# Kernel optimization log

Hardware: AMD Instinct MI355X
Metric: run time of the kernel (lower is better)

## Reference

```python
import jax, jax.numpy as jnp
import numpy as np

B, S, E, H = 1, 2048, 1024, 16
D = E // H  # head_dim = 64


def setup_inputs() -> dict:
    key = jax.random.key(0)
    ks = jax.random.split(key, 9)
    sd = 0.02
    hidden_states = jax.random.normal(ks[0], (B, S, E), dtype=jnp.float32)
    # causal mask: positions with mask==0 are filled with -inf (per masked_fill_)
    mask = jnp.tril(jnp.ones((1, 1, S, S), dtype=bool))
    Wq = jax.random.normal(ks[1], (E, E), dtype=jnp.float32) * sd
    bq = jax.random.normal(ks[2], (E,), dtype=jnp.float32) * sd
    Wk = jax.random.normal(ks[3], (D, E), dtype=jnp.float32) * sd
    bk = jax.random.normal(ks[4], (D,), dtype=jnp.float32) * sd
    Wv = jax.random.normal(ks[5], (D, E), dtype=jnp.float32) * sd
    bv = jax.random.normal(ks[6], (D,), dtype=jnp.float32) * sd
    Wo = jax.random.normal(ks[7], (E, E), dtype=jnp.float32) * sd
    bo = jax.random.normal(ks[8], (E,), dtype=jnp.float32) * sd
    return {"hidden_states": hidden_states, "mask": mask,
            "Wq": Wq, "bq": bq, "Wk": Wk, "bk": bk,
            "Wv": Wv, "bv": bv, "Wo": Wo, "bo": bo}


def reference(hidden_states, mask, Wq, bq, Wk, bk, Wv, bv, Wo, bo):
    bsz, tgt_len, embed_dim = hidden_states.shape
    # projections (torch Linear: x @ W^T + b)
    q = hidden_states @ Wq.T + bq                       # [B, S, E]
    q = q.reshape(bsz, tgt_len, H, D).transpose(0, 2, 1, 3)  # [B, H, S, D]
    k = hidden_states @ Wk.T + bk                       # [B, S, D] shared single KV head
    v = hidden_states @ Wv.T + bv                       # [B, S, D]
    scaling = jnp.sqrt(jnp.asarray(D, dtype=hidden_states.dtype))
    # QK^T with implicit broadcast of the shared K head (instead of expand)
    scores = jnp.einsum('bhqd,bkd->bhqk', q, k) / scaling   # [B, H, S, S]
    scores = jnp.where(mask, scores, -jnp.inf)
    probs = jax.nn.softmax(scores, axis=-1)             # dropout p=0 -> identity
    attn = jnp.einsum('bhqk,bkd->bhqd', probs, v)       # [B, H, S, D]
    attn = attn.transpose(0, 2, 1, 3).reshape(bsz, tgt_len, H * D)
    return attn @ Wo.T + bo                             # [B, S, E]
```

## Files before the change

### kernel.cpp

```cpp
#include <hip/hip_runtime.h>
#include <hip/hip_bf16.h>

typedef __hip_bfloat16 bf16;
typedef __attribute__((ext_vector_type(8))) short short8;
typedef __attribute__((ext_vector_type(4))) float f32x4;

__device__ __forceinline__ short8 ld8(const void* p) { return *(const short8*)p; }

__device__ __forceinline__ void async_cp16(bf16* lds, const bf16* g) {
    __builtin_amdgcn_global_load_lds(
        (const __attribute__((address_space(1))) unsigned int*)g,
        (__attribute__((address_space(3))) unsigned int*)lds, 16, 0, 0);
}

struct bf4 { bf16 a, b, c, d; };

__global__ void cast_kernel(const float* __restrict__ s0, bf16* __restrict__ d0, int n0_,
                            const float* __restrict__ s1, bf16* __restrict__ d1, int n1_,
                            const float* __restrict__ s2, bf16* __restrict__ d2, int n2_,
                            const float* __restrict__ s3, bf16* __restrict__ d3, int n3_,
                            const float* __restrict__ s4, bf16* __restrict__ d4, int n4_) {
    const float* srcs[5] = {s0, s1, s2, s3, s4};
    bf16* dsts[5] = {d0, d1, d2, d3, d4};
    int ns[5] = {n0_, n1_, n2_, n3_, n4_};
    int stride = gridDim.x * blockDim.x;
    int t0 = blockIdx.x * blockDim.x + threadIdx.x;
#pragma unroll
    for (int a = 0; a < 5; ++a) {
        const float4* src = (const float4*)srcs[a];
        bf4* dst = (bf4*)dsts[a];
        int n4 = ns[a] >> 2;
        for (int i = t0; i < n4; i += stride) {
            float4 v = src[i];
            bf4 o = {__float2bfloat16(v.x), __float2bfloat16(v.y),
                     __float2bfloat16(v.z), __float2bfloat16(v.w)};
            dst[i] = o;
        }
    }
}

#define GEMM_STAGE(dst, src_base, row0, ldk)                                   \
    _Pragma("unroll")                                                          \
    for (int u = 0; u < 4; ++u) {                                              \
        int t = wave * 4 + u;                                                  \
        int row = t * 4 + (lane >> 4);                                         \
        int gsrc = (lane & 15) ^ (row & 15);                                   \
        async_cp16(&dst[t * 4][0], src_base + (size_t)(row0 + row) * ldk + k0 + gsrc * 8); \
    }

__global__ void qkv_proj_kernel(const bf16* __restrict__ A,
                                const bf16* __restrict__ Wq, const bf16* __restrict__ Wk,
                                const bf16* __restrict__ Wv,
                                const float* __restrict__ bq, const float* __restrict__ bk,
                                const float* __restrict__ bv,
                                bf16* __restrict__ qo, bf16* __restrict__ ko,
                                bf16* __restrict__ vto, int M, int K) {
    __shared__ __align__(16) bf16 As[64][128];
    __shared__ __align__(16) bf16 Bs[64][128];
    const int nt = blockIdx.x;
    const bf16* W;
    const float* bias;
    int mode, nw0;
    if (nt < 16)      { W = Wq; bias = bq; mode = 0; nw0 = nt * 64; }
    else if (nt == 16){ W = Wk; bias = bk; mode = 1; nw0 = 0; }
    else              { W = Wv; bias = bv; mode = 2; nw0 = 0; }

    const int tid = threadIdx.x;
    const int wave = tid >> 6, lane = tid & 63;
    const int l16 = lane & 15, quad = lane >> 4;
    const int m0 = blockIdx.y * 64;

    f32x4 acc[4];
    const f32x4 z = {0.f, 0.f, 0.f, 0.f};
#pragma unroll
    for (int ni = 0; ni < 4; ++ni) acc[ni] = z;

    for (int k0 = 0; k0 < K; k0 += 128) {
        GEMM_STAGE(As, A, m0, K)
        GEMM_STAGE(Bs, W, nw0, K)
        __syncthreads();

        short8 af[4], bfr[4][4];
        {
            int R = wave * 16 + l16;
#pragma unroll
            for (int kc = 0; kc < 4; ++kc)
                af[kc] = ld8(&As[R][((kc * 4 + quad) ^ (R & 15)) * 8]);
        }
#pragma unroll
        for (int ni = 0; ni < 4; ++ni) {
            int r = ni * 16 + l16;
#pragma unroll
            for (int kc = 0; kc < 4; ++kc)
                bfr[kc][ni] = ld8(&Bs[r][((kc * 4 + quad) ^ (r & 15)) * 8]);
        }
#pragma unroll
        for (int kc = 0; kc < 4; ++kc)
#pragma unroll
            for (int ni = 0; ni < 4; ++ni)
                acc[ni] = __builtin_amdgcn_mfma_f32_16x16x32_bf16(
                    af[kc], bfr[kc][ni], acc[ni], 0, 0, 0);
        __syncthreads();
    }

#pragma unroll
    for (int ni = 0; ni < 4; ++ni)
#pragma unroll
        for (int r = 0; r < 4; ++r) {
            int row = m0 + wave * 16 + quad * 4 + r;
            int col = ni * 16 + l16;
            float v = acc[ni][r] + bias[nw0 + col];
            if (mode == 0)
                qo[(size_t)row * 1024 + nt * 64 + col] = __float2bfloat16(v * 0.125f);
            else if (mode == 1)
                ko[(size_t)row * 64 + col] = __float2bfloat16(v);
            else
                vto[(size_t)col * M + row] = __float2bfloat16(v);
        }
}

__global__ void gemm_bt_mfma(const bf16* __restrict__ A, const bf16* __restrict__ W,
                             const float* __restrict__ bias, float* __restrict__ C,
                             int M, int N, int K) {
    __shared__ __align__(16) bf16 As[64][128];
    __shared__ __align__(16) bf16 Bs[64][128];
    const int tid = threadIdx.x;
    const int wave = tid >> 6, lane = tid & 63;
    const int l16 = lane & 15, quad = lane >> 4;
    const int m0 = blockIdx.y * 64, n0 = blockIdx.x * 64;

    f32x4 acc[4];
    const f32x4 z = {0.f, 0.f, 0.f, 0.f};
#pragma unroll
    for (int ni = 0; ni < 4; ++ni) acc[ni] = z;

    for (int k0 = 0; k0 < K; k0 += 128) {
        GEMM_STAGE(As, A, m0, K)
        GEMM_STAGE(Bs, W, n0, K)
        __syncthreads();

        short8 af[4], bfr[4][4];
        {
            int R = wave * 16 + l16;
#pragma unroll
            for (int kc = 0; kc < 4; ++kc)
                af[kc] = ld8(&As[R][((kc * 4 + quad) ^ (R & 15)) * 8]);
        }
#pragma unroll
        for (int ni = 0; ni < 4; ++ni) {
            int r = ni * 16 + l16;
#pragma unroll
            for (int kc = 0; kc < 4; ++kc)
                bfr[kc][ni] = ld8(&Bs[r][((kc * 4 + quad) ^ (r & 15)) * 8]);
        }
#pragma unroll
        for (int kc = 0; kc < 4; ++kc)
#pragma unroll
            for (int ni = 0; ni < 4; ++ni)
                acc[ni] = __builtin_amdgcn_mfma_f32_16x16x32_bf16(
                    af[kc], bfr[kc][ni], acc[ni], 0, 0, 0);
        __syncthreads();
    }

#pragma unroll
    for (int ni = 0; ni < 4; ++ni)
#pragma unroll
        for (int r = 0; r < 4; ++r) {
            int row = m0 + wave * 16 + quad * 4 + r;
            int col = n0 + ni * 16 + l16;
            C[(size_t)row * N + col] = acc[ni][r] + bias[col];
        }
}

__global__ void flash_mfma_kernel(const bf16* __restrict__ Q, const bf16* __restrict__ Kg,
                                  const bf16* __restrict__ VT,
                                  bf16* __restrict__ Opart, float* __restrict__ Lpart,
                                  bf16* __restrict__ attn, int S) {
    const int s = blockIdx.x;
    int i, c;
    if (s < 32)      { c = 0; i = s; }
    else if (s < 56) { c = 1; i = s - 24; }
    else if (s < 72) { c = 2; i = s - 40; }
    else             { c = 3; i = s - 48; }

    __shared__ __align__(16) bf16 Ks[64][64];
    __shared__ __align__(16) bf16 Vt[64][64];
    __shared__ bf16 Ps[4][16][68];

    const int h = blockIdx.y;
    const int q0 = i * 64;
    const int tid = threadIdx.x;
    const int wave = tid >> 6, lane = tid & 63;
    const int l16 = lane & 15, quad = lane >> 4;
    const int lr = lane >> 3, lsw = (lane & 7) ^ (lr & 7);
    const int qrow = q0 + wave * 16;

    short8 qf[2];
#pragma unroll
    for (int kc = 0; kc < 2; ++kc)
        qf[kc] = ld8(Q + (size_t)(qrow + l16) * 1024 + h * 64 + kc * 32 + quad * 8);

    short8 onesf;
    {
        short o = (l16 == 0) ? (short)0x3F80 : (short)0;
        onesf[0]=o; onesf[1]=o; onesf[2]=o; onesf[3]=o;
        onesf[4]=o; onesf[5]=o; onesf[6]=o; onesf[7]=o;
    }

    f32x4 of[4];
    const f32x4 z = {0.f, 0.f, 0.f, 0.f};
#pragma unroll
    for (int dt = 0; dt < 4; ++dt) of[dt] = z;
    f32x4 lacc = z;

    const int jt0 = c * 8;
    const int jt1 = min(c * 8 + 8, i + 1);

    for (int jt = jt0; jt < jt1; ++jt) {
        const int j0 = jt * 64;
#pragma unroll
        for (int u = 0; u < 2; ++u) {
            int t = wave * 2 + u;
            async_cp16(&Ks[t * 8][0], Kg + (size_t)(j0 + t * 8 + lr) * 64 + lsw * 8);
            async_cp16(&Vt[t * 8][0], VT + (size_t)(t * 8 + lr) * S + j0 + lsw * 8);
        }
        __syncthreads();

        f32x4 sc[4];
#pragma unroll
        for (int nt = 0; nt < 4; ++nt) {
            int R = nt * 16 + l16;
            sc[nt] = __builtin_amdgcn_mfma_f32_16x16x32_bf16(
                qf[0], ld8(&Ks[R][(quad ^ (R & 7)) * 8]), z, 0, 0, 0);
            sc[nt] = __builtin_amdgcn_mfma_f32_16x16x32_bf16(
                qf[1], ld8(&Ks[R][((4 + quad) ^ (R & 7)) * 8]), sc[nt], 0, 0, 0);
        }
        bool need_mask = (j0 + 63 > qrow);
        if (need_mask) {
#pragma unroll
            for (int nt = 0; nt < 4; ++nt)
#pragma unroll
                for (int r = 0; r < 4; ++r)
                    if (j0 + nt * 16 + l16 > qrow + quad * 4 + r) sc[nt][r] = -1e30f;
        }

#pragma unroll
        for (int nt = 0; nt < 4; ++nt)
#pragma unroll
            for (int r = 0; r < 4; ++r)
                Ps[wave][quad * 4 + r][nt * 16 + l16] = __float2bfloat16(__expf(sc[nt][r]));

        short8 pf[2];
        pf[0] = ld8(&Ps[wave][l16][quad * 8]);
        pf[1] = ld8(&Ps[wave][l16][32 + quad * 8]);

        lacc = __builtin_amdgcn_mfma_f32_16x16x32_bf16(pf[0], onesf, lacc, 0, 0, 0);
        lacc = __builtin_amdgcn_mfma_f32_16x16x32_bf16(pf[1], onesf, lacc, 0, 0, 0);

#pragma unroll
        for (int dt = 0; dt < 4; ++dt) {
            int R = dt * 16 + l16;
            of[dt] = __builtin_amdgcn_mfma_f32_16x16x32_bf16(
                pf[0], ld8(&Vt[R][(quad ^ (R & 7)) * 8]), of[dt], 0, 0, 0);
            of[dt] = __builtin_amdgcn_mfma_f32_16x16x32_bf16(
                pf[1], ld8(&Vt[R][((4 + quad) ^ (R & 7)) * 8]), of[dt], 0, 0, 0);
        }
        __syncthreads();
    }

    if (s < 8) {
        float inv[4];
#pragma unroll
        for (int r = 0; r < 4; ++r)
            inv[r] = 1.f / __shfl(lacc[r], quad * 16);
#pragma unroll
        for (int dt = 0; dt < 4; ++dt)
#pragma unroll
            for (int r = 0; r < 4; ++r) {
                int row = q0 + wave * 16 + quad * 4 + r;
                attn[(size_t)row * 1024 + h * 64 + dt * 16 + l16] =
                    __float2bfloat16(of[dt][r] * inv[r]);
            }
        return;
    }

    bf16* Op = Opart + ((size_t)s * 16 + h) * 4096;
#pragma unroll
    for (int dt = 0; dt < 4; ++dt)
#pragma unroll
        for (int r = 0; r < 4; ++r) {
            int row = wave * 16 + quad * 4 + r;
            Op[row * 64 + dt * 16 + l16] = __float2bfloat16(of[dt][r]);
        }
    if (l16 == 0) {
        float* L = Lpart + ((size_t)s * 16 + h) * 64;
#pragma unroll
        for (int r = 0; r < 4; ++r)
            L[wave * 16 + quad * 4 + r] = lacc[r];
    }
}

__global__ void flash_merge_kernel(const bf16* __restrict__ Opart,
                                   const float* __restrict__ Lpart,
                                   bf16* __restrict__ attn) {
    const int i = blockIdx.x + 8, h = blockIdx.y;
    const int nch = (i >> 3) + 1;
    const int tid = threadIdx.x;
    const int row = tid >> 2, cg = (tid & 3) * 16;

    float L = 0.f;
    for (int cc = 0; cc < nch; ++cc) {
        int s = (cc == 0) ? i : (cc == 1) ? 24 + i : (cc == 2) ? 40 + i : 48 + i;
        L += Lpart[((size_t)s * 16 + h) * 64 + row];
    }
    float inv = 1.f / L;

    float o[16];
#pragma unroll
    for (int j = 0; j < 16; ++j) o[j] = 0.f;
    for (int cc = 0; cc < nch; ++cc) {
        int s = (cc == 0) ? i : (cc == 1) ? 24 + i : (cc == 2) ? 40 + i : 48 + i;
        const bf16* Op = Opart + ((size_t)s * 16 + h) * 4096 + row * 64 + cg;
#pragma unroll
        for (int j = 0; j < 16; ++j) o[j] += __bfloat162float(Op[j]);
    }
    bf16* dst = attn + (size_t)(i * 64 + row) * 1024 + h * 64 + cg;
#pragma unroll
    for (int j = 0; j < 16; ++j) dst[j] = __float2bfloat16(o[j] * inv);
}

extern "C" void kernel_launch(void* const* d_in, const int* in_sizes, int n_in,
                              void* d_out, int out_size, void* d_ws, size_t ws_size,
                              hipStream_t stream) {
    const int S = 2048, E = 1024, D = 64;

    const float* hs = (const float*)d_in[0];
    const float* Wq = (const float*)d_in[2];
    const float* bq = (const float*)d_in[3];
    const float* Wk = (const float*)d_in[4];
    const float* bk = (const float*)d_in[5];
    const float* Wv = (const float*)d_in[6];
    const float* bv = (const float*)d_in[7];
    const float* Wo = (const float*)d_in[8];
    const float* bo = (const float*)d_in[9];
    float* out = (float*)d_out;

    bf16* ws = (bf16*)d_ws;
    bf16* hsb = ws;
    bf16* wqb = hsb + (size_t)S * E;
    bf16* wkb = wqb + (size_t)E * E;
    bf16* wvb = wkb + (size_t)D * E;
    bf16* wob = wvb + (size_t)D * E;
    bf16* q = wob + (size_t)E * E;
    bf16* kbuf = q + (size_t)S * E;
    bf16* vt = kbuf + (size_t)S * D;
    bf16* attn = vt + (size_t)S * D;
    bf16* Opart = attn + (size_t)S * E;
    float* Lpart = (float*)(Opart + (size_t)1280 * 4096);

    cast_kernel<<<512, 256, 0, stream>>>(hs, hsb, S * E,
                                         Wq, wqb, E * E,
                                         Wk, wkb, D * E,
                                         Wv, wvb, D * E,
                                         Wo, wob, E * E);
    qkv_proj_kernel<<<dim3(18, S / 64), 256, 0, stream>>>(hsb, wqb, wkb, wvb,
                                                          bq, bk, bv,
                                                          q, kbuf, vt, S, E);
    flash_mfma_kernel<<<dim3(80, 16), 256, 0, stream>>>(q, kbuf, vt, Opart, Lpart, attn, S);
    flash_merge_kernel<<<dim3(24, 16), 256, 0, stream>>>(Opart, Lpart, attn);
    gemm_bt_mfma<<<dim3(E / 64, S / 64), 256, 0, stream>>>(attn, wob, bo, out, S, E, E);
}
```

Baseline: 147.9 us.

## Double-buffer LDS and widen N tile to 128 in projection GEMMs

Both projection GEMMs now double-buffer the A and B LDS tiles, so the next K slice is loaded asynchronously while MFMAs run on the current one. The N tile grows from 64 to 128 and each wave computes a 32x64 sub-tile, which raises operand reuse from LDS. The QKV kernel merges the K and V heads into one 128-wide tile. The cost is more LDS per block (96KB) and more accumulator registers, and the grids shrink to 9x32 and 8x32 blocks, which may underfill the CUs.

```diff
diff --git a/kernel.cpp b/kernel.cpp
--- a/kernel.cpp
+++ b/kernel.cpp
@@ -39,14 +39,31 @@
     }
 }
 
-#define GEMM_STAGE(dst, src_base, row0, ldk)                                   \
-    _Pragma("unroll")                                                          \
-    for (int u = 0; u < 4; ++u) {                                              \
-        int t = wave * 4 + u;                                                  \
-        int row = t * 4 + (lane >> 4);                                         \
-        int gsrc = (lane & 15) ^ (row & 15);                                   \
-        async_cp16(&dst[t * 4][0], src_base + (size_t)(row0 + row) * ldk + k0 + gsrc * 8); \
-    }
+template<int NROWS>
+__device__ __forceinline__ void stage_tile(bf16 (*dst)[128], const bf16* src,
+                                           int ldk, int wave, int lane) {
+#pragma unroll
+    for (int u = 0; u < NROWS / 16; ++u) {
+        int t = wave * (NROWS / 16) + u;
+        int row = t * 4 + (lane >> 4);
+        int gsrc = (lane & 15) ^ (row & 15);
+        async_cp16(&dst[t * 4][0], src + (size_t)row * ldk + gsrc * 8);
+    }
+}
+
+__device__ __forceinline__ void stage_kv(bf16 (*dst)[128], const bf16* Wk,
+                                         const bf16* Wv, int k0, int K,
+                                         int wave, int lane) {
+#pragma unroll
+    for (int u = 0; u < 8; ++u) {
+        int t = wave * 8 + u;
+        int row = t * 4 + (lane >> 4);
+        const bf16* src = (t < 16) ? (Wk + (size_t)row * K)
+                                   : (Wv + (size_t)(row - 64) * K);
+        int gsrc = (lane & 15) ^ (row & 15);
+        async_cp16(&dst[t * 4][0], src + k0 + gsrc * 8);
+    }
+}
 
 __global__ void qkv_proj_kernel(const bf16* __restrict__ A,
                                 const bf16* __restrict__ Wq, const bf16* __restrict__ Wk,
@@ -55,121 +72,152 @@
                                 const float* __restrict__ bv,
                                 bf16* __restrict__ qo, bf16* __restrict__ ko,
                                 bf16* __restrict__ vto, int M, int K) {
-    __shared__ __align__(16) bf16 As[64][128];
-    __shared__ __align__(16) bf16 Bs[64][128];
+    __shared__ __align__(16) bf16 As[2][64][128];
+    __shared__ __align__(16) bf16 Bs[2][128][128];
     const int nt = blockIdx.x;
-    const bf16* W;
-    const float* bias;
-    int mode, nw0;
-    if (nt < 16)      { W = Wq; bias = bq; mode = 0; nw0 = nt * 64; }
-    else if (nt == 16){ W = Wk; bias = bk; mode = 1; nw0 = 0; }
-    else              { W = Wv; bias = bv; mode = 2; nw0 = 0; }
-
+    const int m0 = blockIdx.y * 64;
     const int tid = threadIdx.x;
     const int wave = tid >> 6, lane = tid & 63;
     const int l16 = lane & 15, quad = lane >> 4;
-    const int m0 = blockIdx.y * 64;
-
-    f32x4 acc[4];
+    const int wr = wave >> 1, wc = wave & 1;
+
+    f32x4 acc[2][4];
     const f32x4 z = {0.f, 0.f, 0.f, 0.f};
 #pragma unroll
-    for (int ni = 0; ni < 4; ++ni) acc[ni] = z;
-
-    for (int k0 = 0; k0 < K; k0 += 128) {
-        GEMM_STAGE(As, A, m0, K)
-        GEMM_STAGE(Bs, W, nw0, K)
+    for (int mi = 0; mi < 2; ++mi)
+#pragma unroll
+        for (int ni = 0; ni < 4; ++ni) acc[mi][ni] = z;
+
+    const int nk = K / 128;
+    stage_tile<64>(As[0], A + (size_t)m0 * K, K, wave, lane);
+    if (nt < 8) stage_tile<128>(Bs[0], Wq + (size_t)(nt * 128) * K, K, wave, lane);
+    else        stage_kv(Bs[0], Wk, Wv, 0, K, wave, lane);
+    __syncthreads();
+
+    for (int kt = 0; kt < nk; ++kt) {
+        const int cur = kt & 1;
+        if (kt + 1 < nk) {
+            const int k0 = (kt + 1) * 128;
+            stage_tile<64>(As[cur ^ 1], A + (size_t)m0 * K + k0, K, wave, lane);
+            if (nt < 8)
+                stage_tile<128>(Bs[cur ^ 1], Wq + (size_t)(nt * 128) * K + k0, K, wave, lane);
+            else
+                stage_kv(Bs[cur ^ 1], Wk, Wv, k0, K, wave, lane);
+        }
+        short8 af[2][4], bfr[4][4];
+#pragma unroll
+        for (int mi = 0; mi < 2; ++mi) {
+            int R = wr * 32 + mi * 16 + l16;
+#pragma unroll
+            for (int kc = 0; kc < 4; ++kc)
+                af[mi][kc] = ld8(&As[cur][R][((kc * 4 + quad) ^ (R & 15)) * 8]);
+        }
+#pragma unroll
+        for (int ni = 0; ni < 4; ++ni) {
+            int r = wc * 64 + ni * 16 + l16;
+#pragma unroll
+            for (int kc = 0; kc < 4; ++kc)
+                bfr[ni][kc] = ld8(&Bs[cur][r][((kc * 4 + quad) ^ (r & 15)) * 8]);
+        }
+#pragma unroll
+        for (int kc = 0; kc < 4; ++kc)
+#pragma unroll
+            for (int mi = 0; mi < 2; ++mi)
+#pragma unroll
+                for (int ni = 0; ni < 4; ++ni)
+                    acc[mi][ni] = __builtin_amdgcn_mfma_f32_16x16x32_bf16(
+                        af[mi][kc], bfr[ni][kc], acc[mi][ni], 0, 0, 0);
         __syncthreads();
-
-        short8 af[4], bfr[4][4];
-        {
-            int R = wave * 16 + l16;
-#pragma unroll
-            for (int kc = 0; kc < 4; ++kc)
-                af[kc] = ld8(&As[R][((kc * 4 + quad) ^ (R & 15)) * 8]);
-        }
-#pragma unroll
-        for (int ni = 0; ni < 4; ++ni) {
-            int r = ni * 16 + l16;
-#pragma unroll
-            for (int kc = 0; kc < 4; ++kc)
-                bfr[kc][ni] = ld8(&Bs[r][((kc * 4 + quad) ^ (r & 15)) * 8]);
-        }
-#pragma unroll
-        for (int kc = 0; kc < 4; ++kc)
-#pragma unroll
-            for (int ni = 0; ni < 4; ++ni)
-                acc[ni] = __builtin_amdgcn_mfma_f32_16x16x32_bf16(
-                    af[kc], bfr[kc][ni], acc[ni], 0, 0, 0);
-        __syncthreads();
-    }
-
-#pragma unroll
-    for (int ni = 0; ni < 4; ++ni)
-#pragma unroll
-        for (int r = 0; r < 4; ++r) {
-            int row = m0 + wave * 16 + quad * 4 + r;
-            int col = ni * 16 + l16;
-            float v = acc[ni][r] + bias[nw0 + col];
-            if (mode == 0)
-                qo[(size_t)row * 1024 + nt * 64 + col] = __float2bfloat16(v * 0.125f);
-            else if (mode == 1)
-                ko[(size_t)row * 64 + col] = __float2bfloat16(v);
-            else
-                vto[(size_t)col * M + row] = __float2bfloat16(v);
-        }
+    }
+
+#pragma unroll
+    for (int mi = 0; mi < 2; ++mi)
+#pragma unroll
+        for (int ni = 0; ni < 4; ++ni)
+#pragma unroll
+            for (int r = 0; r < 4; ++r) {
+                int row = m0 + wr * 32 + mi * 16 + quad * 4 + r;
+                int c = wc * 64 + ni * 16 + l16;
+                float v = acc[mi][ni][r];
+                if (nt < 8) {
+                    int col = nt * 128 + c;
+                    qo[(size_t)row * 1024 + col] =
+                        __float2bfloat16((v + bq[col]) * 0.125f);
+                } else if (c < 64) {
+                    ko[(size_t)row * 64 + c] = __float2bfloat16(v + bk[c]);
+                } else {
+                    vto[(size_t)(c - 64) * M + row] =
+                        __float2bfloat16(v + bv[c - 64]);
+                }
+            }
 }
 
 __global__ void gemm_bt_mfma(const bf16* __restrict__ A, const bf16* __restrict__ W,
                              const float* __restrict__ bias, float* __restrict__ C,
                              int M, int N, int K) {
-    __shared__ __align__(16) bf16 As[64][128];
-    __shared__ __align__(16) bf16 Bs[64][128];
+    __shared__ __align__(16) bf16 As[2][64][128];
+    __shared__ __align__(16) bf16 Bs[2][128][128];
     const int tid = threadIdx.x;
     const int wave = tid >> 6, lane = tid & 63;
     const int l16 = lane & 15, quad = lane >> 4;
-    const int m0 = blockIdx.y * 64, n0 = blockIdx.x * 64;
-
-    f32x4 acc[4];
+    const int wr = wave >> 1, wc = wave & 1;
+    const int m0 = blockIdx.y * 64, n0 = blockIdx.x * 128;
+
+    f32x4 acc[2][4];
     const f32x4 z = {0.f, 0.f, 0.f, 0.f};
 #pragma unroll
-    for (int ni = 0; ni < 4; ++ni) acc[ni] = z;
-
-    for (int k0 = 0; k0 < K; k0 += 128) {
-        GEMM_STAGE(As, A, m0, K)
-        GEMM_STAGE(Bs, W, n0, K)
+    for (int mi = 0; mi < 2; ++mi)
+#pragma unroll
+        for (int ni = 0; ni < 4; ++ni) acc[mi][ni] = z;
+
+    const int nk = K / 128;
+    stage_tile<64>(As[0], A + (size_t)m0 * K, K, wave, lane);
+    stage_tile<128>(Bs[0], W + (size_t)n0 * K, K, wave, lane);
+    __syncthreads();
+
+    for (int kt = 0; kt < nk; ++kt) {
+        const int cur = kt & 1;
+        if (kt + 1 < nk) {
+            const int k0 = (kt + 1) * 128;
+            stage_tile<64>(As[cur ^ 1], A + (size_t)m0 * K + k0, K, wave, lane);
+            stage_tile<128>(Bs[cur ^ 1], W + (size_t)n0 * K + k0, K, wave, lane);
+        }
+        short8 af[2][4], bfr[4][4];
+#pragma unroll
+        for (int mi = 0; mi < 2; ++mi) {
+            int R = wr * 32 + mi * 16 + l16;
+#pragma unroll
+            for (int kc = 0; kc < 4; ++kc)
+                af[mi][kc] = ld8(&As[cur][R][((kc * 4 + quad) ^ (R & 15)) * 8]);
+        }
+#pragma unroll
+        for (int ni = 0; ni < 4; ++ni) {
+            int r = wc * 64 + ni * 16 + l16;
+#pragma unroll
+            for (int kc = 0; kc < 4; ++kc)
+                bfr[ni][kc] = ld8(&Bs[cur][r][((kc * 4 + quad) ^ (r & 15)) * 8]);
+        }
+#pragma unroll
+        for (int kc = 0; kc < 4; ++kc)
+#pragma unroll
+            for (int mi = 0; mi < 2; ++mi)
+#pragma unroll
+                for (int ni = 0; ni < 4; ++ni)
+                    acc[mi][ni] = __builtin_amdgcn_mfma_f32_16x16x32_bf16(
+                        af[mi][kc], bfr[ni][kc], acc[mi][ni], 0, 0, 0);
         __syncthreads();
-
-        short8 af[4], bfr[4][4];
-        {
-            int R = wave * 16 + l16;
-#pragma unroll
-            for (int kc = 0; kc < 4; ++kc)
-                af[kc] = ld8(&As[R][((kc * 4 + quad) ^ (R & 15)) * 8]);
-        }
-#pragma unroll
-        for (int ni = 0; ni < 4; ++ni) {
-            int r = ni * 16 + l16;
-#pragma unroll
-            for (int kc = 0; kc < 4; ++kc)
-                bfr[kc][ni] = ld8(&Bs[r][((kc * 4 + quad) ^ (r & 15)) * 8]);
-        }
-#pragma unroll
-        for (int kc = 0; kc < 4; ++kc)
-#pragma unroll
-            for (int ni = 0; ni < 4; ++ni)
-                acc[ni] = __builtin_amdgcn_mfma_f32_16x16x32_bf16(
-                    af[kc], bfr[kc][ni], acc[ni], 0, 0, 0);
-        __syncthreads();
-    }
-
-#pragma unroll
-    for (int ni = 0; ni < 4; ++ni)
-#pragma unroll
-        for (int r = 0; r < 4; ++r) {
-            int row = m0 + wave * 16 + quad * 4 + r;
-            int col = n0 + ni * 16 + l16;
-            C[(size_t)row * N + col] = acc[ni][r] + bias[col];
-        }
+    }
+
+#pragma unroll
+    for (int mi = 0; mi < 2; ++mi)
+#pragma unroll
+        for (int ni = 0; ni < 4; ++ni)
+#pragma unroll
+            for (int r = 0; r < 4; ++r) {
+                int row = m0 + wr * 32 + mi * 16 + quad * 4 + r;
+                int col = n0 + wc * 64 + ni * 16 + l16;
+                C[(size_t)row * N + col] = acc[mi][ni][r] + bias[col];
+            }
 }
 
 __global__ void flash_mfma_kernel(const bf16* __restrict__ Q, const bf16* __restrict__ Kg,
@@ -363,10 +411,10 @@
                                          Wk, wkb, D * E,
                                          Wv, wvb, D * E,
                                          Wo, wob, E * E);
-    qkv_proj_kernel<<<dim3(18, S / 64), 256, 0, stream>>>(hsb, wqb, wkb, wvb,
-                                                          bq, bk, bv,
-                                                          q, kbuf, vt, S, E);
+    qkv_proj_kernel<<<dim3(9, S / 64), 256, 0, stream>>>(hsb, wqb, wkb, wvb,
+                                                         bq, bk, bv,
+                                                         q, kbuf, vt, S, E);
     flash_mfma_kernel<<<dim3(80, 16), 256, 0, stream>>>(q, kbuf, vt, Opart, Lpart, attn, S);
     flash_merge_kernel<<<dim3(24, 16), 256, 0, stream>>>(Opart, Lpart, attn);
-    gemm_bt_mfma<<<dim3(E / 64, S / 64), 256, 0, stream>>>(attn, wob, bo, out, S, E, E);
-}
+    gemm_bt_mfma<<<dim3(E / 128, S / 64), 256, 0, stream>>>(attn, wob, bo, out, S, E, E);
+}
```

Measured after the change: 162.9 us. 10.1% more time.

## Double-buffer KV tiles in flash kernel and use 2x2 wave tiling in GEMMs

Applied to the files above, without the earlier changes.

The flash attention loop now stages K/V tiles into a second LDS buffer while the current tile is being computed, aiming to hide global-to-LDS load latency. Both GEMM kernels switch from one wave per 16-row strip computing all 64 columns to a 2x2 wave arrangement where each wave computes a 32x32 sub-tile, which cuts per-wave LDS fragment reads for B. The double buffering doubles K/V LDS usage. The next tile's async loads are issued before compute with only the end-of-iteration barrier, which may leave the LDS writes not yet visible when that buffer is read, since no explicit wait for the async copies is shown.

```diff
diff --git a/kernel.cpp b/kernel.cpp
--- a/kernel.cpp
+++ b/kernel.cpp
@@ -68,55 +68,63 @@
     const int tid = threadIdx.x;
     const int wave = tid >> 6, lane = tid & 63;
     const int l16 = lane & 15, quad = lane >> 4;
+    const int wr = wave >> 1, wc = wave & 1;
     const int m0 = blockIdx.y * 64;
 
-    f32x4 acc[4];
+    f32x4 acc[2][2];
     const f32x4 z = {0.f, 0.f, 0.f, 0.f};
 #pragma unroll
-    for (int ni = 0; ni < 4; ++ni) acc[ni] = z;
+    for (int mi = 0; mi < 2; ++mi)
+#pragma unroll
+        for (int ni = 0; ni < 2; ++ni) acc[mi][ni] = z;
 
     for (int k0 = 0; k0 < K; k0 += 128) {
         GEMM_STAGE(As, A, m0, K)
         GEMM_STAGE(Bs, W, nw0, K)
         __syncthreads();
 
-        short8 af[4], bfr[4][4];
-        {
-            int R = wave * 16 + l16;
+        short8 af[2][4], bfr[2][4];
+#pragma unroll
+        for (int mi = 0; mi < 2; ++mi) {
+            int R = wr * 32 + mi * 16 + l16;
 #pragma unroll
             for (int kc = 0; kc < 4; ++kc)
-                af[kc] = ld8(&As[R][((kc * 4 + quad) ^ (R & 15)) * 8]);
-        }
-#pragma unroll
-        for (int ni = 0; ni < 4; ++ni) {
-            int r = ni * 16 + l16;
+                af[mi][kc] = ld8(&As[R][((kc * 4 + quad) ^ (R & 15)) * 8]);
+        }
+#pragma unroll
+        for (int ni = 0; ni < 2; ++ni) {
+            int r = wc * 32 + ni * 16 + l16;
 #pragma unroll
             for (int kc = 0; kc < 4; ++kc)
-                bfr[kc][ni] = ld8(&Bs[r][((kc * 4 + quad) ^ (r & 15)) * 8]);
+                bfr[ni][kc] = ld8(&Bs[r][((kc * 4 + quad) ^ (r & 15)) * 8]);
         }
 #pragma unroll
         for (int kc = 0; kc < 4; ++kc)
 #pragma unroll
-            for (int ni = 0; ni < 4; ++ni)
-                acc[ni] = __builtin_amdgcn_mfma_f32_16x16x32_bf16(
-                    af[kc], bfr[kc][ni], acc[ni], 0, 0, 0);
+            for (int mi = 0; mi < 2; ++mi)
+#pragma unroll
+                for (int ni = 0; ni < 2; ++ni)
+                    acc[mi][ni] = __builtin_amdgcn_mfma_f32_16x16x32_bf16(
+                        af[mi][kc], bfr[ni][kc], acc[mi][ni], 0, 0, 0);
         __syncthreads();
     }
 
 #pragma unroll
-    for (int ni = 0; ni < 4; ++ni)
-#pragma unroll
-        for (int r = 0; r < 4; ++r) {
-            int row = m0 + wave * 16 + quad * 4 + r;
-            int col = ni * 16 + l16;
-            float v = acc[ni][r] + bias[nw0 + col];
-            if (mode == 0)
-                qo[(size_t)row * 1024 + nt * 64 + col] = __float2bfloat16(v * 0.125f);
-            else if (mode == 1)
-                ko[(size_t)row * 64 + col] = __float2bfloat16(v);
-            else
-                vto[(size_t)col * M + row] = __float2bfloat16(v);
-        }
+    for (int mi = 0; mi < 2; ++mi)
+#pragma unroll
+        for (int ni = 0; ni < 2; ++ni)
+#pragma unroll
+            for (int r = 0; r < 4; ++r) {
+                int row = m0 + wr * 32 + mi * 16 + quad * 4 + r;
+                int c = wc * 32 + ni * 16 + l16;
+                float v = acc[mi][ni][r] + bias[nw0 + c];
+                if (mode == 0)
+                    qo[(size_t)row * 1024 + nt * 64 + c] = __float2bfloat16(v * 0.125f);
+                else if (mode == 1)
+                    ko[(size_t)row * 64 + c] = __float2bfloat16(v);
+                else
+                    vto[(size_t)c * M + row] = __float2bfloat16(v);
+            }
 }
 
 __global__ void gemm_bt_mfma(const bf16* __restrict__ A, const bf16* __restrict__ W,
@@ -127,49 +135,57 @@
     const int tid = threadIdx.x;
     const int wave = tid >> 6, lane = tid & 63;
     const int l16 = lane & 15, quad = lane >> 4;
+    const int wr = wave >> 1, wc = wave & 1;
     const int m0 = blockIdx.y * 64, n0 = blockIdx.x * 64;
 
-    f32x4 acc[4];
+    f32x4 acc[2][2];
     const f32x4 z = {0.f, 0.f, 0.f, 0.f};
 #pragma unroll
-    for (int ni = 0; ni < 4; ++ni) acc[ni] = z;
+    for (int mi = 0; mi < 2; ++mi)
+#pragma unroll
+        for (int ni = 0; ni < 2; ++ni) acc[mi][ni] = z;
 
     for (int k0 = 0; k0 < K; k0 += 128) {
         GEMM_STAGE(As, A, m0, K)
         GEMM_STAGE(Bs, W, n0, K)
         __syncthreads();
 
-        short8 af[4], bfr[4][4];
-        {
-            int R = wave * 16 + l16;
+        short8 af[2][4], bfr[2][4];
+#pragma unroll
+        for (int mi = 0; mi < 2; ++mi) {
+            int R = wr * 32 + mi * 16 + l16;
 #pragma unroll
             for (int kc = 0; kc < 4; ++kc)
-                af[kc] = ld8(&As[R][((kc * 4 + quad) ^ (R & 15)) * 8]);
-        }
-#pragma unroll
-        for (int ni = 0; ni < 4; ++ni) {
-            int r = ni * 16 + l16;
+                af[mi][kc] = ld8(&As[R][((kc * 4 + quad) ^ (R & 15)) * 8]);
+        }
+#pragma unroll
+        for (int ni = 0; ni < 2; ++ni) {
+            int r = wc * 32 + ni * 16 + l16;
 #pragma unroll
             for (int kc = 0; kc < 4; ++kc)
-                bfr[kc][ni] = ld8(&Bs[r][((kc * 4 + quad) ^ (r & 15)) * 8]);
+                bfr[ni][kc] = ld8(&Bs[r][((kc * 4 + quad) ^ (r & 15)) * 8]);
         }
 #pragma unroll
         for (int kc = 0; kc < 4; ++kc)
 #pragma unroll
-            for (int ni = 0; ni < 4; ++ni)
-                acc[ni] = __builtin_amdgcn_mfma_f32_16x16x32_bf16(
-                    af[kc], bfr[kc][ni], acc[ni], 0, 0, 0);
+            for (int mi = 0; mi < 2; ++mi)
+#pragma unroll
+                for (int ni = 0; ni < 2; ++ni)
+                    acc[mi][ni] = __builtin_amdgcn_mfma_f32_16x16x32_bf16(
+                        af[mi][kc], bfr[ni][kc], acc[mi][ni], 0, 0, 0);
         __syncthreads();
     }
 
 #pragma unroll
-    for (int ni = 0; ni < 4; ++ni)
-#pragma unroll
-        for (int r = 0; r < 4; ++r) {
-            int row = m0 + wave * 16 + quad * 4 + r;
-            int col = n0 + ni * 16 + l16;
-            C[(size_t)row * N + col] = acc[ni][r] + bias[col];
-        }
+    for (int mi = 0; mi < 2; ++mi)
+#pragma unroll
+        for (int ni = 0; ni < 2; ++ni)
+#pragma unroll
+            for (int r = 0; r < 4; ++r) {
+                int row = m0 + wr * 32 + mi * 16 + quad * 4 + r;
+                int col = n0 + wc * 32 + ni * 16 + l16;
+                C[(size_t)row * N + col] = acc[mi][ni][r] + bias[col];
+            }
 }
 
 __global__ void flash_mfma_kernel(const bf16* __restrict__ Q, const bf16* __restrict__ Kg,
@@ -183,8 +199,8 @@
     else if (s < 72) { c = 2; i = s - 40; }
     else             { c = 3; i = s - 48; }
 
-    __shared__ __align__(16) bf16 Ks[64][64];
-    __shared__ __align__(16) bf16 Vt[64][64];
+    __shared__ __align__(16) bf16 Ks[2][64][64];
+    __shared__ __align__(16) bf16 Vt[2][64][64];
     __shared__ bf16 Ps[4][16][68];
 
     const int h = blockIdx.y;
@@ -215,25 +231,38 @@
 
     const int jt0 = c * 8;
     const int jt1 = min(c * 8 + 8, i + 1);
-
-    for (int jt = jt0; jt < jt1; ++jt) {
+    const int nits = jt1 - jt0;
+
+#define STAGE_KV(buf, jt_)                                                       \
+    do {                                                                         \
+        const int j0_ = (jt_) * 64;                                              \
+        _Pragma("unroll")                                                        \
+        for (int u = 0; u < 2; ++u) {                                            \
+            int t = wave * 2 + u;                                                \
+            async_cp16(&Ks[buf][t * 8][0],                                       \
+                       Kg + (size_t)(j0_ + t * 8 + lr) * 64 + lsw * 8);          \
+            async_cp16(&Vt[buf][t * 8][0],                                       \
+                       VT + (size_t)(t * 8 + lr) * S + j0_ + lsw * 8);           \
+        }                                                                        \
+    } while (0)
+
+    STAGE_KV(0, jt0);
+    __syncthreads();
+
+    for (int it = 0; it < nits; ++it) {
+        const int jt = jt0 + it;
         const int j0 = jt * 64;
-#pragma unroll
-        for (int u = 0; u < 2; ++u) {
-            int t = wave * 2 + u;
-            async_cp16(&Ks[t * 8][0], Kg + (size_t)(j0 + t * 8 + lr) * 64 + lsw * 8);
-            async_cp16(&Vt[t * 8][0], VT + (size_t)(t * 8 + lr) * S + j0 + lsw * 8);
-        }
-        __syncthreads();
+        const int cur = it & 1;
+        if (it + 1 < nits) STAGE_KV(cur ^ 1, jt + 1);
 
         f32x4 sc[4];
 #pragma unroll
         for (int nt = 0; nt < 4; ++nt) {
             int R = nt * 16 + l16;
             sc[nt] = __builtin_amdgcn_mfma_f32_16x16x32_bf16(
-                qf[0], ld8(&Ks[R][(quad ^ (R & 7)) * 8]), z, 0, 0, 0);
+                qf[0], ld8(&Ks[cur][R][(quad ^ (R & 7)) * 8]), z, 0, 0, 0);
             sc[nt] = __builtin_amdgcn_mfma_f32_16x16x32_bf16(
-                qf[1], ld8(&Ks[R][((4 + quad) ^ (R & 7)) * 8]), sc[nt], 0, 0, 0);
+                qf[1], ld8(&Ks[cur][R][((4 + quad) ^ (R & 7)) * 8]), sc[nt], 0, 0, 0);
         }
         bool need_mask = (j0 + 63 > qrow);
         if (need_mask) {
@@ -261,12 +290,13 @@
         for (int dt = 0; dt < 4; ++dt) {
             int R = dt * 16 + l16;
             of[dt] = __builtin_amdgcn_mfma_f32_16x16x32_bf16(
-                pf[0], ld8(&Vt[R][(quad ^ (R & 7)) * 8]), of[dt], 0, 0, 0);
+                pf[0], ld8(&Vt[cur][R][(quad ^ (R & 7)) * 8]), of[dt], 0, 0, 0);
             of[dt] = __builtin_amdgcn_mfma_f32_16x16x32_bf16(
-                pf[1], ld8(&Vt[R][((4 + quad) ^ (R & 7)) * 8]), of[dt], 0, 0, 0);
+                pf[1], ld8(&Vt[cur][R][((4 + quad) ^ (R & 7)) * 8]), of[dt], 0, 0, 0);
         }
         __syncthreads();
     }
+#undef STAGE_KV
 
     if (s < 8) {
         float inv[4];
```

After: 148.3 us. No clear change (+0.3%).
